# Performance work log

Hardware: AMD Instinct MI355X
Metric: run time of the kernel (lower is better)

The kernel has to match this reference:

```python
import jax, jax.numpy as jnp
from jax import lax
import numpy as np

N_QUBITS = 10  # min(dim, n_wires) wires carry RX gates; rest stay |0>


def setup_inputs() -> dict:
    key = jax.random.key(0)
    k1, k2, k3, k4 = jax.random.split(key, 4)
    T, B, D, H, C = 128, 512, 512, 512, 32
    inputs = jax.random.normal(k1, (T, B, D), dtype=jnp.float32)
    # 4 gates (f, i, g, o), centres init ~ 0.1 * randn as in the module
    centres = 0.1 * jax.random.normal(k2, (4, C, D + H), dtype=jnp.float32)
    lin_w = jax.random.normal(k3, (4, H, C), dtype=jnp.float32) / jnp.sqrt(jnp.float32(C))
    lin_b = jax.random.normal(k4, (4, H), dtype=jnp.float32) * 0.01
    return {"inputs": inputs, "centres": centres, "lin_w": lin_w, "lin_b": lin_b}


def _quantum_kernel(comb, ctr):
    # comb: [B, dim], ctr: [C, dim]
    # Circuit = RX(x_i) then RX(-y_i) on wire i (i < N_QUBITS) => RX(x_i - y_i).
    # |<0..0|state>| = prod_i |cos((x_i - y_i)/2)| over active wires.
    m = min(comb.shape[-1], N_QUBITS)
    diff = comb[:, None, :m] - ctr[None, :, :m]  # [B, C, m]
    return jnp.prod(jnp.abs(jnp.cos(0.5 * diff)), axis=-1)  # [B, C]


def reference(inputs, centres, lin_w, lin_b):
    T, B, D = inputs.shape
    H = lin_w.shape[1]
    h0 = jnp.zeros((B, H), dtype=inputs.dtype)
    c0 = jnp.zeros((B, H), dtype=inputs.dtype)

    def step(carry, x):
        h, c = carry
        comb = jnp.concatenate([x, h], axis=1)  # [B, D+H]
        # kernels for all 4 gates at once: [4, B, C]
        k = jax.vmap(lambda ct: _quantum_kernel(comb, ct))(centres)
        pre = jnp.einsum('gbc,ghc->gbh', k, lin_w) + lin_b[:, None, :]  # [4, B, H]
        f = jax.nn.sigmoid(pre[0])
        i = jax.nn.sigmoid(pre[1])
        g = jnp.tanh(pre[2])
        o = jax.nn.sigmoid(pre[3])
        c_new = f * c + i * g
        h_new = o * jnp.tanh(c_new)
        return (h_new, c_new), h_new

    (h, c), outputs = lax.scan(step, (h0, c0), inputs)
    return outputs, h, c
```

## Files before the change

kernel.cpp:

```cpp
#include <hip/hip_runtime.h>

#define TT 128
#define BB 512
#define DD 512
#define HH 512
#define CC 32
#define NQ 10
#define GC 128
#define DH 1024
#define CHUNK 16
#define NCHUNK (TT / CHUNK)

typedef __fp16 h2 __attribute__((ext_vector_type(2)));
typedef __fp16 h4 __attribute__((ext_vector_type(4)));
typedef __fp16 h8 __attribute__((ext_vector_type(8)));
typedef float f4 __attribute__((ext_vector_type(4)));

__device__ __forceinline__ float rcpf(float x) {
    return __builtin_amdgcn_rcpf(x);
}
__device__ __forceinline__ float sigmf(float x) {
    return rcpf(1.f + __expf(-x));
}
__device__ __forceinline__ float tanhfast(float x) {
    return 1.f - 2.f * rcpf(1.f + __expf(2.f * x));
}

__global__ __launch_bounds__(512, 2) void qlstm_kernel(
    const float* __restrict__ inputs,
    const float* __restrict__ centres,
    const float* __restrict__ lin_w,
    const float* __restrict__ lin_b,
    float* __restrict__ out)
{
    __shared__ __fp16 Klds[TT * GC];
    __shared__ __fp16 pre[CHUNK * HH * 4];
    __shared__ float xs[TT * NQ];
    __shared__ float cs[GC * NQ];

    const int b = blockIdx.x;
    const int tid = threadIdx.x;
    const int lane = tid & 63;
    const int w = tid >> 6;

    h8 bfr[16];
    {
        const int c0 = (lane >> 4) * 8;
        #pragma unroll
        for (int g = 0; g < 4; ++g) {
            #pragma unroll
            for (int j = 0; j < 4; ++j) {
                const int hcol = (w * 4 + j) * 16 + (lane & 15);
                const float* wp = lin_w + (((size_t)g * HH + hcol) * CC + c0);
                f4 lo = *(const f4*)wp;
                f4 hi = *(const f4*)(wp + 4);
                h2 p0 = __builtin_amdgcn_cvt_pkrtz(lo.x, lo.y);
                h2 p1 = __builtin_amdgcn_cvt_pkrtz(lo.z, lo.w);
                h2 p2 = __builtin_amdgcn_cvt_pkrtz(hi.x, hi.y);
                h2 p3 = __builtin_amdgcn_cvt_pkrtz(hi.z, hi.w);
                h8 bb = { p0.x, p0.y, p1.x, p1.y, p2.x, p2.y, p3.x, p3.y };
                bfr[g * 4 + j] = bb;
            }
        }
    }

    const float bias0 = lin_b[0 * HH + tid];
    const float bias1 = lin_b[1 * HH + tid];
    const float bias2 = lin_b[2 * HH + tid];
    const float bias3 = lin_b[3 * HH + tid];

    for (int idx = tid; idx < TT * NQ; idx += 512) {
        int t = idx / NQ, q = idx - t * NQ;
        xs[idx] = inputs[((size_t)t * BB + b) * DD + q];
    }
    for (int idx = tid; idx < GC * NQ; idx += 512) {
        int gc = idx / NQ, q = idx - gc * NQ;
        cs[idx] = centres[(size_t)gc * DH + q];
    }
    __syncthreads();

    for (int v = tid; v < TT * GC; v += 512) {
        int t = v >> 7, gc = v & 127;
        const float* xr = &xs[t * NQ];
        const float* cr = &cs[gc * NQ];
        float p = 1.f;
        #pragma unroll
        for (int q = 0; q < NQ; ++q)
            p *= fabsf(__cosf(0.5f * (xr[q] - cr[q])));
        Klds[v] = (__fp16)p;
    }
    __syncthreads();

    float cstate = 0.f, hstate = 0.f;
    float* op = out + (size_t)b * HH + tid;
    const f4 z4 = {0.f, 0.f, 0.f, 0.f};

    for (int ct = 0; ct < NCHUNK; ++ct) {
        const int arow = ct * CHUNK + (lane & 15);
        h8 afr[4];
        #pragma unroll
        for (int g = 0; g < 4; ++g)
            afr[g] = *(const h8*)&Klds[arow * GC + g * 32 + (lane >> 4) * 8];

        #pragma unroll
        for (int j = 0; j < 4; ++j) {
            f4 a0 = __builtin_amdgcn_mfma_f32_16x16x32_f16(afr[0], bfr[0 * 4 + j], z4, 0, 0, 0);
            f4 a1 = __builtin_amdgcn_mfma_f32_16x16x32_f16(afr[1], bfr[1 * 4 + j], z4, 0, 0, 0);
            f4 a2 = __builtin_amdgcn_mfma_f32_16x16x32_f16(afr[2], bfr[2 * 4 + j], z4, 0, 0, 0);
            f4 a3 = __builtin_amdgcn_mfma_f32_16x16x32_f16(afr[3], bfr[3 * 4 + j], z4, 0, 0, 0);
            const int hcol = (w * 4 + j) * 16 + (lane & 15);
            #pragma unroll
            for (int r = 0; r < 4; ++r) {
                const int tl = (lane >> 4) * 4 + r;
                h2 p01 = __builtin_amdgcn_cvt_pkrtz(a0[r], a1[r]);
                h2 p23 = __builtin_amdgcn_cvt_pkrtz(a2[r], a3[r]);
                h4 pv = { p01.x, p01.y, p23.x, p23.y };
                *(h4*)&pre[((size_t)tl * HH + hcol) * 4] = pv;
            }
        }
        __syncthreads();

        #pragma unroll
        for (int tl = 0; tl < CHUNK; ++tl) {
            h4 v = *(const h4*)&pre[((size_t)tl * HH + tid) * 4];
            float af = bias0 + (float)v.x;
            float ai = bias1 + (float)v.y;
            float ag = bias2 + (float)v.z;
            float ao = bias3 + (float)v.w;
            float fg = sigmf(af);
            float ig = sigmf(ai);
            float gg = tanhfast(ag);
            float og = sigmf(ao);
            cstate = fg * cstate + ig * gg;
            hstate = og * tanhfast(cstate);
            op[(size_t)(ct * CHUNK + tl) * (BB * HH)] = hstate;
        }
        __syncthreads();
    }

    float* hout = out + (size_t)TT * BB * HH;
    float* cout = hout + (size_t)BB * HH;
    hout[(size_t)b * HH + tid] = hstate;
    cout[(size_t)b * HH + tid] = cstate;
}

extern "C" void kernel_launch(void* const* d_in, const int* in_sizes, int n_in,
                              void* d_out, int out_size, void* d_ws, size_t ws_size,
                              hipStream_t stream) {
    const float* inputs  = (const float*)d_in[0];
    const float* centres = (const float*)d_in[1];
    const float* lin_w   = (const float*)d_in[2];
    const float* lin_b   = (const float*)d_in[3];
    float* out = (float*)d_out;

    qlstm_kernel<<<dim3(BB), dim3(512), 0, stream>>>(inputs, centres, lin_w, lin_b, out);
}
```

Before: 97.06 us.

## Halve recurrence chunk, raise occupancy, fold bias into MFMA, swizzle LDS

Shrinks the per-chunk time window from 16 to 8 steps so the pre-activation LDS buffer is halved, and raises the launch-bounds occupancy hint from 2 to 4 blocks per CU. The bias is folded into the MFMA accumulator init. The K table and pre-activation buffers use XOR-swizzled layouts to avoid bank conflicts, and the kernel table is written four halves at a time. Only half the MFMA rows are used with CHUNK 8, which wastes matrix throughput. The tighter register budget may also cause spills.

```diff
diff --git a/kernel.cpp b/kernel.cpp
--- a/kernel.cpp
+++ b/kernel.cpp
@@ -8,7 +8,7 @@
 #define NQ 10
 #define GC 128
 #define DH 1024
-#define CHUNK 16
+#define CHUNK 8
 #define NCHUNK (TT / CHUNK)
 
 typedef __fp16 h2 __attribute__((ext_vector_type(2)));
@@ -26,7 +26,7 @@
     return 1.f - 2.f * rcpf(1.f + __expf(2.f * x));
 }
 
-__global__ __launch_bounds__(512, 2) void qlstm_kernel(
+__global__ __launch_bounds__(512, 4) void qlstm_kernel(
     const float* __restrict__ inputs,
     const float* __restrict__ centres,
     const float* __restrict__ lin_w,
@@ -34,7 +34,8 @@
     float* __restrict__ out)
 {
     __shared__ __fp16 Klds[TT * GC];
-    __shared__ __fp16 pre[CHUNK * HH * 4];
+    __shared__ unsigned pre_fi[CHUNK * HH];
+    __shared__ unsigned pre_go[CHUNK * HH];
     __shared__ float xs[TT * NQ];
     __shared__ float cs[GC * NQ];
 
@@ -42,15 +43,18 @@
     const int tid = threadIdx.x;
     const int lane = tid & 63;
     const int w = tid >> 6;
+    const int q = lane >> 4;
+    const int c16 = lane & 15;
 
     h8 bfr[16];
+    float biasv[16];
     {
-        const int c0 = (lane >> 4) * 8;
+        const int c0 = q * 8;
         #pragma unroll
         for (int g = 0; g < 4; ++g) {
             #pragma unroll
             for (int j = 0; j < 4; ++j) {
-                const int hcol = (w * 4 + j) * 16 + (lane & 15);
+                const int hcol = (w * 4 + j) * 16 + c16;
                 const float* wp = lin_w + (((size_t)g * HH + hcol) * CC + c0);
                 f4 lo = *(const f4*)wp;
                 f4 hi = *(const f4*)(wp + 4);
@@ -60,77 +64,91 @@
                 h2 p3 = __builtin_amdgcn_cvt_pkrtz(hi.z, hi.w);
                 h8 bb = { p0.x, p0.y, p1.x, p1.y, p2.x, p2.y, p3.x, p3.y };
                 bfr[g * 4 + j] = bb;
+                biasv[g * 4 + j] = lin_b[g * HH + hcol];
             }
         }
     }
 
-    const float bias0 = lin_b[0 * HH + tid];
-    const float bias1 = lin_b[1 * HH + tid];
-    const float bias2 = lin_b[2 * HH + tid];
-    const float bias3 = lin_b[3 * HH + tid];
-
     for (int idx = tid; idx < TT * NQ; idx += 512) {
-        int t = idx / NQ, q = idx - t * NQ;
-        xs[idx] = inputs[((size_t)t * BB + b) * DD + q];
+        int t = idx / NQ, qq = idx - t * NQ;
+        xs[idx] = inputs[((size_t)t * BB + b) * DD + qq];
     }
     for (int idx = tid; idx < GC * NQ; idx += 512) {
-        int gc = idx / NQ, q = idx - gc * NQ;
-        cs[idx] = centres[(size_t)gc * DH + q];
+        int gc = idx / NQ, qq = idx - gc * NQ;
+        cs[idx] = centres[(size_t)gc * DH + qq];
     }
     __syncthreads();
 
-    for (int v = tid; v < TT * GC; v += 512) {
-        int t = v >> 7, gc = v & 127;
+    for (int p = 0; p < 8; ++p) {
+        int idx = tid + p * 512;
+        int t = idx >> 5, gc0 = (idx & 31) * 4;
         const float* xr = &xs[t * NQ];
-        const float* cr = &cs[gc * NQ];
-        float p = 1.f;
+        float pv[4];
         #pragma unroll
-        for (int q = 0; q < NQ; ++q)
-            p *= fabsf(__cosf(0.5f * (xr[q] - cr[q])));
-        Klds[v] = (__fp16)p;
+        for (int u = 0; u < 4; ++u) {
+            const float* cr = &cs[(gc0 + u) * NQ];
+            float pr = 1.f;
+            #pragma unroll
+            for (int qq = 0; qq < NQ; ++qq)
+                pr *= fabsf(__cosf(0.5f * (xr[qq] - cr[qq])));
+            pv[u] = pr;
+        }
+        h2 lo2 = __builtin_amdgcn_cvt_pkrtz(pv[0], pv[1]);
+        h2 hi2 = __builtin_amdgcn_cvt_pkrtz(pv[2], pv[3]);
+        h4 kk = { lo2.x, lo2.y, hi2.x, hi2.y };
+        int byteo = (t * 256 + gc0 * 2) ^ ((t & 7) << 4);
+        *(h4*)((char*)Klds + byteo) = kk;
     }
     __syncthreads();
 
     float cstate = 0.f, hstate = 0.f;
     float* op = out + (size_t)b * HH + tid;
-    const f4 z4 = {0.f, 0.f, 0.f, 0.f};
+    const int tlo = c16 & 7;
 
     for (int ct = 0; ct < NCHUNK; ++ct) {
-        const int arow = ct * CHUNK + (lane & 15);
+        const int arow = ct * CHUNK + tlo;
         h8 afr[4];
         #pragma unroll
         for (int g = 0; g < 4; ++g)
-            afr[g] = *(const h8*)&Klds[arow * GC + g * 32 + (lane >> 4) * 8];
+            afr[g] = *(const h8*)((const char*)Klds +
+                     ((arow * 256 + g * 64 + q * 16) ^ ((arow & 7) << 4)));
 
         #pragma unroll
         for (int j = 0; j < 4; ++j) {
-            f4 a0 = __builtin_amdgcn_mfma_f32_16x16x32_f16(afr[0], bfr[0 * 4 + j], z4, 0, 0, 0);
-            f4 a1 = __builtin_amdgcn_mfma_f32_16x16x32_f16(afr[1], bfr[1 * 4 + j], z4, 0, 0, 0);
-            f4 a2 = __builtin_amdgcn_mfma_f32_16x16x32_f16(afr[2], bfr[2 * 4 + j], z4, 0, 0, 0);
-            f4 a3 = __builtin_amdgcn_mfma_f32_16x16x32_f16(afr[3], bfr[3 * 4 + j], z4, 0, 0, 0);
-            const int hcol = (w * 4 + j) * 16 + (lane & 15);
-            #pragma unroll
-            for (int r = 0; r < 4; ++r) {
-                const int tl = (lane >> 4) * 4 + r;
-                h2 p01 = __builtin_amdgcn_cvt_pkrtz(a0[r], a1[r]);
-                h2 p23 = __builtin_amdgcn_cvt_pkrtz(a2[r], a3[r]);
-                h4 pv = { p01.x, p01.y, p23.x, p23.y };
-                *(h4*)&pre[((size_t)tl * HH + hcol) * 4] = pv;
+            f4 c0 = { biasv[0*4+j], biasv[0*4+j], biasv[0*4+j], biasv[0*4+j] };
+            f4 c1 = { biasv[1*4+j], biasv[1*4+j], biasv[1*4+j], biasv[1*4+j] };
+            f4 c2 = { biasv[2*4+j], biasv[2*4+j], biasv[2*4+j], biasv[2*4+j] };
+            f4 c3 = { biasv[3*4+j], biasv[3*4+j], biasv[3*4+j], biasv[3*4+j] };
+            f4 a0 = __builtin_amdgcn_mfma_f32_16x16x32_f16(afr[0], bfr[0*4+j], c0, 0, 0, 0);
+            f4 a1 = __builtin_amdgcn_mfma_f32_16x16x32_f16(afr[1], bfr[1*4+j], c1, 0, 0, 0);
+            f4 a2 = __builtin_amdgcn_mfma_f32_16x16x32_f16(afr[2], bfr[2*4+j], c2, 0, 0, 0);
+            f4 a3 = __builtin_amdgcn_mfma_f32_16x16x32_f16(afr[3], bfr[3*4+j], c3, 0, 0, 0);
+            if (q < 2) {
+                const int hcol = (w * 4 + j) * 16 + c16;
+                #pragma unroll
+                for (int r = 0; r < 4; ++r) {
+                    const int tl = q * 4 + r;
+                    h2 p01 = __builtin_amdgcn_cvt_pkrtz(a0[r], a1[r]);
+                    h2 p23 = __builtin_amdgcn_cvt_pkrtz(a2[r], a3[r]);
+                    const int colw = hcol ^ (q << 4);
+                    pre_fi[tl * HH + colw] = *(unsigned*)&p01;
+                    pre_go[tl * HH + colw] = *(unsigned*)&p23;
+                }
             }
         }
         __syncthreads();
 
         #pragma unroll
         for (int tl = 0; tl < CHUNK; ++tl) {
-            h4 v = *(const h4*)&pre[((size_t)tl * HH + tid) * 4];
-            float af = bias0 + (float)v.x;
-            float ai = bias1 + (float)v.y;
-            float ag = bias2 + (float)v.z;
-            float ao = bias3 + (float)v.w;
-            float fg = sigmf(af);
-            float ig = sigmf(ai);
-            float gg = tanhfast(ag);
-            float og = sigmf(ao);
+            const int colr = tid ^ ((tl & 4) << 2);
+            unsigned ufi = pre_fi[tl * HH + colr];
+            unsigned ugo = pre_go[tl * HH + colr];
+            h2 vfi = *(h2*)&ufi;
+            h2 vgo = *(h2*)&ugo;
+            float fg = sigmf((float)vfi.x);
+            float ig = sigmf((float)vfi.y);
+            float gg = tanhfast((float)vgo.x);
+            float og = sigmf((float)vgo.y);
             cstate = fg * cstate + ig * gg;
             hstate = og * tanhfast(cstate);
             op[(size_t)(ct * CHUNK + tl) * (BB * HH)] = hstate;
```

New measurement: 222.7 us. 129% more time.
